# Kernel optimization log

Hardware: AMD Instinct MI355X
Metric: run time of the kernel (lower is better)

## Reference

```python
import jax, jax.numpy as jnp
import numpy as np

DIM = 1024
INTER = 512
E = 16            # n_routed_experts
TOPK = 4          # n_activated_experts
N_GROUPS = 4
TOPK_GROUPS = 2
ROUTE_SCALE = 1.0
INIT_STD = 0.02
B, S = 2, 1024


def setup_inputs() -> dict:
    key = jax.random.key(0)
    ks = jax.random.split(key, 8)
    return {
        "x": jax.random.normal(ks[0], (B, S, DIM), jnp.float32),
        "gate_w": jax.random.normal(ks[1], (E, DIM), jnp.float32) * INIT_STD,
        "gate_bias": jnp.zeros((E,), jnp.float32),
        "w1": jax.random.normal(ks[2], (E, INTER, DIM), jnp.float32) * INIT_STD,
        "w2": jax.random.normal(ks[3], (E, DIM, INTER), jnp.float32) * INIT_STD,
        "w3": jax.random.normal(ks[4], (E, INTER, DIM), jnp.float32) * INIT_STD,
        "ws1": jax.random.normal(ks[5], (INTER, DIM), jnp.float32) * INIT_STD,
        "ws2": jax.random.normal(ks[6], (DIM, INTER), jnp.float32) * INIT_STD,
        "ws3": jax.random.normal(ks[7], (INTER, DIM), jnp.float32) * INIT_STD,
    }


def reference(x, gate_w, gate_bias, w1, w2, w3, ws1, ws2, ws3):
    Bx, Sx, D = x.shape
    T = Bx * Sx
    xf = x.reshape(T, D)

    # ---- Gate: sigmoid scores + expert bias, group-limited top-k ----
    scores = jax.nn.sigmoid(xf @ gate_w.T)          # [T, E]
    original_scores = scores
    s = scores + gate_bias                          # bias only affects selection
    sg = s.reshape(T, N_GROUPS, E // N_GROUPS)
    group_scores = sg.max(axis=-1)                  # [T, G]
    _, gidx = jax.lax.top_k(group_scores, TOPK_GROUPS)
    keep = jnp.zeros((T, N_GROUPS), bool).at[jnp.arange(T)[:, None], gidx].set(True)
    s_masked = jnp.where(keep[:, :, None], sg, -jnp.inf).reshape(T, E)
    _, idx = jax.lax.top_k(s_masked, TOPK)          # [T, topk]
    weights = jnp.take_along_axis(original_scores, idx, axis=1) * ROUTE_SCALE

    # combine weights as sparse [T, E] matrix (scatter of top-k weights)
    comb = jnp.zeros((T, E), x.dtype).at[jnp.arange(T)[:, None], idx].add(weights)

    # ---- Routed experts: SwiGLU per expert, weighted combine ----
    h1 = jnp.einsum('td,eid->tei', xf, w1)          # [T, E, inter]
    h3 = jnp.einsum('td,eid->tei', xf, w3)
    h = jax.nn.silu(h1) * h3
    y = jnp.einsum('tei,edi,te->td', h, w2, comb)   # weighted combine

    # ---- Shared expert (SwiGLU MLP) ----
    z = (jax.nn.silu(xf @ ws1.T) * (xf @ ws3.T)) @ ws2.T

    return (y + z).reshape(Bx, Sx, D)
```

## Files before the change

### kernel.cpp

```cpp
#include <hip/hip_runtime.h>

#define T_TOK  2048
#define DIMD   1024
#define INTERI 512
#define NEXP   16
#define NSEG   17

typedef __bf16 bf16x8 __attribute__((ext_vector_type(8)));
typedef float  f32x4  __attribute__((ext_vector_type(4)));
typedef unsigned short u16x8 __attribute__((ext_vector_type(8)));

#define SW(row, c) ((((c) + ((row) >> 1)) & 3) * 8)

__device__ __forceinline__ unsigned short f2b(float f) {
    union { float f; unsigned int u; } c; c.f = f;
    unsigned int u = c.u;
    unsigned int r = (u + 0x7FFFu + ((u >> 16) & 1u)) >> 16;
    return (unsigned short)r;
}

__device__ __forceinline__ void glds16(const void* g, void* l) {
    __builtin_amdgcn_global_load_lds(
        (const __attribute__((address_space(1))) unsigned int*)g,
        (__attribute__((address_space(3))) unsigned int*)l,
        16, 0, 0);
}

__device__ __forceinline__ void dma_barrier() {
    asm volatile("s_waitcnt vmcnt(0)" ::: "memory");
    __syncthreads();
}

__global__ __launch_bounds__(256) void prep_kernel(
    const float* __restrict__ w1,  const float* __restrict__ w3,
    const float* __restrict__ w2,
    const float* __restrict__ ws1, const float* __restrict__ ws3,
    const float* __restrict__ ws2,
    unsigned short* __restrict__ w1b,  unsigned short* __restrict__ w3b,
    unsigned short* __restrict__ w2b,
    unsigned short* __restrict__ ws1b, unsigned short* __restrict__ ws3b,
    unsigned short* __restrict__ ws2b,
    const float* __restrict__ x, const float* __restrict__ gw,
    const float* __restrict__ gb,
    unsigned* __restrict__ sel, float4* __restrict__ selw,
    unsigned short* __restrict__ xb)
{
    const int b = blockIdx.x;
    if (b >= 512) {
        int g = (b - 512) * 256 + threadIdx.x;
        const float* s; unsigned short* d; int i;
        if      (g < 524288)  { s = w1;  d = w1b;  i = g; }
        else if (g < 1048576) { s = w3;  d = w3b;  i = g - 524288; }
        else if (g < 1572864) { s = w2;  d = w2b;  i = g - 1048576; }
        else if (g < 1605632) { s = ws1; d = ws1b; i = g - 1572864; }
        else if (g < 1638400) { s = ws3; d = ws3b; i = g - 1605632; }
        else                  { s = ws2; d = ws2b; i = g - 1638400; }
        const f32x4* sp = (const f32x4*)s;
        f32x4 v0 = __builtin_nontemporal_load(&sp[4 * i]);
        f32x4 v1 = __builtin_nontemporal_load(&sp[4 * i + 1]);
        f32x4 v2 = __builtin_nontemporal_load(&sp[4 * i + 2]);
        f32x4 v3 = __builtin_nontemporal_load(&sp[4 * i + 3]);
        u16x8 o0, o1;
        o0[0] = f2b(v0[0]); o0[1] = f2b(v0[1]); o0[2] = f2b(v0[2]); o0[3] = f2b(v0[3]);
        o0[4] = f2b(v1[0]); o0[5] = f2b(v1[1]); o0[6] = f2b(v1[2]); o0[7] = f2b(v1[3]);
        o1[0] = f2b(v2[0]); o1[1] = f2b(v2[1]); o1[2] = f2b(v2[2]); o1[3] = f2b(v2[3]);
        o1[4] = f2b(v3[0]); o1[5] = f2b(v3[1]); o1[6] = f2b(v3[2]); o1[7] = f2b(v3[3]);
        ((u16x8*)d)[2 * i]     = o0;
        ((u16x8*)d)[2 * i + 1] = o1;
        return;
    }
    int tok  = b * 4 + (threadIdx.x >> 6);
    int lane = threadIdx.x & 63;
    const float* xp = x + (size_t)tok * DIMD;
    float xv[16];
#pragma unroll
    for (int j = 0; j < 16; ++j) xv[j] = xp[j * 64 + lane];

    unsigned short* xbp = xb + (size_t)tok * DIMD;
#pragma unroll
    for (int j = 0; j < 16; ++j) xbp[j * 64 + lane] = f2b(xv[j]);

    float sc[16];
#pragma unroll
    for (int e = 0; e < 16; ++e) {
        const float* gwe = gw + e * DIMD;
        float p0 = 0.f, p1 = 0.f;
#pragma unroll
        for (int j = 0; j < 16; j += 2) {
            p0 += xv[j]     * gwe[j * 64 + lane];
            p1 += xv[j + 1] * gwe[(j + 1) * 64 + lane];
        }
        float p = p0 + p1;
#pragma unroll
        for (int o = 32; o; o >>= 1) p += __shfl_xor(p, o, 64);
        sc[e] = p;
    }
    if (lane != 0) return;

    float orig[16], s[16];
#pragma unroll
    for (int e = 0; e < 16; ++e) {
        orig[e] = 1.f / (1.f + expf(-sc[e]));
        s[e] = orig[e] + gb[e];
    }
    float gmax[4];
#pragma unroll
    for (int g = 0; g < 4; ++g) {
        float m = s[4 * g];
        for (int j = 1; j < 4; ++j) m = fmaxf(m, s[4 * g + j]);
        gmax[g] = m;
    }
    int g0 = 0;
    for (int g = 1; g < 4; ++g) if (gmax[g] > gmax[g0]) g0 = g;
    int g1 = -1;
    for (int g = 0; g < 4; ++g) { if (g == g0) continue; if (g1 < 0 || gmax[g] > gmax[g1]) g1 = g; }
    unsigned keep = (0xFu << (4 * g0)) | (0xFu << (4 * g1));
    unsigned used = 0;
    unsigned pk = 0;
    float w4[4];
    for (int j = 0; j < 4; ++j) {
        int best = -1;
        for (int e = 0; e < 16; ++e) {
            if (!((keep >> e) & 1u) || ((used >> e) & 1u)) continue;
            if (best < 0 || s[e] > s[best]) best = e;
        }
        used |= 1u << best;
        pk |= ((unsigned)best) << (4 * j);
        w4[j] = orig[best];
    }
    sel[tok] = pk;
    selw[tok] = make_float4(w4[0], w4[1], w4[2], w4[3]);
}

__global__ __launch_bounds__(256) void build_lists_kernel(
    const unsigned* __restrict__ sel, const float4* __restrict__ selw,
    int* __restrict__ counts, int* __restrict__ lst, float* __restrict__ lstw)
{
    const int e    = blockIdx.x;
    const int tid  = threadIdx.x;
    const int wave = tid >> 6;
    const int lane = tid & 63;

    __shared__ int wsum[4];
    __shared__ int basev;
    if (tid == 0) basev = 0;
    __syncthreads();

    for (int c = 0; c < T_TOK / 256; ++c) {
        int t = c * 256 + tid;
        unsigned s = sel[t];
        int match = -1;
#pragma unroll
        for (int j = 0; j < 4; ++j)
            if (((s >> (4 * j)) & 15u) == (unsigned)e) match = j;
        unsigned long long m = __ballot(match >= 0);
        int wpre = __popcll(m & ((1ull << lane) - 1ull));
        if (lane == 0) wsum[wave] = __popcll(m);
        __syncthreads();
        int pre = basev;
        for (int wv = 0; wv < wave; ++wv) pre += wsum[wv];
        if (match >= 0) {
            int pos = pre + wpre;
            lst [e * T_TOK + pos] = t | (match << 16);
            const float* wp = (const float*)&selw[t];
            lstw[e * T_TOK + pos] = wp[match];
        }
        __syncthreads();
        if (tid == 0) basev += wsum[0] + wsum[1] + wsum[2] + wsum[3];
        __syncthreads();
    }
    if (tid == 0) counts[e] = basev;
}

__global__ __launch_bounds__(256, 2) void gemm1_kernel(
    const unsigned short* __restrict__ xb,
    const unsigned short* __restrict__ w1b,
    const unsigned short* __restrict__ w3b,
    const unsigned short* __restrict__ ws1b,
    const unsigned short* __restrict__ ws3b,
    const int* __restrict__ counts,
    const int* __restrict__ lst,
    unsigned short* __restrict__ H)
{
    int b = blockIdx.x;
    int seg, mt, nt;
    if (b < 1024) {
        int xcd = b & 7, slot = b >> 3;
        seg = xcd + 8 * (slot >> 6);
        int tile = slot & 63;
        mt = tile >> 2; nt = tile & 3;
    } else {
        seg = NEXP;
        int tile = b - 1024;
        mt = tile >> 2; nt = tile & 3;
    }
    const int n_e = (seg == NEXP) ? T_TOK : counts[seg];
    const int m0  = mt * 128;
    if (m0 >= n_e) return;
    const int n0  = nt * 128;

    const unsigned short* w1p = (seg == NEXP) ? ws1b : w1b + (size_t)seg * INTERI * DIMD;
    const unsigned short* w3p = (seg == NEXP) ? ws3b : w3b + (size_t)seg * INTERI * DIMD;
    const int* lste = lst + seg * T_TOK;

    __shared__ __align__(16) unsigned short lA [2][128][32];
    __shared__ __align__(16) unsigned short lB1[2][128][32];
    __shared__ __align__(16) unsigned short lB3[2][128][32];

    const int tid  = threadIdx.x;
    const int wave = tid >> 6;
    const int lane = tid & 63;
    const int quad = lane >> 4;
    const int lrow = lane & 15;

    const int lr  = lane >> 2;
    const int lsl = lane & 3;
    const int r0  = wave * 32 + lr, r1 = r0 + 16;
    const int c0  = (lsl - (r0 >> 1)) & 3;
    const int c1  = (lsl - (r1 >> 1)) & 3;
    int ga0 = m0 + r0; if (ga0 > n_e - 1) ga0 = n_e - 1;
    int ga1 = m0 + r1; if (ga1 > n_e - 1) ga1 = n_e - 1;
    const int tA0 = (seg == NEXP) ? ga0 : (lste[ga0] & 0xFFFF);
    const int tA1 = (seg == NEXP) ? ga1 : (lste[ga1] & 0xFFFF);
    const unsigned short* pA0  = xb  + (size_t)tA0 * DIMD + c0 * 8;
    const unsigned short* pA1  = xb  + (size_t)tA1 * DIMD + c1 * 8;
    const unsigned short* pB10 = w1p + (size_t)(n0 + r0) * DIMD + c0 * 8;
    const unsigned short* pB11 = w1p + (size_t)(n0 + r1) * DIMD + c1 * 8;
    const unsigned short* pB30 = w3p + (size_t)(n0 + r0) * DIMD + c0 * 8;
    const unsigned short* pB31 = w3p + (size_t)(n0 + r1) * DIMD + c1 * 8;

#define G1STAGE(k0) do { \
    glds16(pA0  + (k0),      &lA [0][wave * 32][0]); \
    glds16(pA0  + (k0) + 32, &lA [1][wave * 32][0]); \
    glds16(pA1  + (k0),      &lA [0][wave * 32 + 16][0]); \
    glds16(pA1  + (k0) + 32, &lA [1][wave * 32 + 16][0]); \
    glds16(pB10 + (k0),      &lB1[0][wave * 32][0]); \
    glds16(pB10 + (k0) + 32, &lB1[1][wave * 32][0]); \
    glds16(pB11 + (k0),      &lB1[0][wave * 32 + 16][0]); \
    glds16(pB11 + (k0) + 32, &lB1[1][wave * 32 + 16][0]); \
    glds16(pB30 + (k0),      &lB3[0][wave * 32][0]); \
    glds16(pB30 + (k0) + 32, &lB3[1][wave * 32][0]); \
    glds16(pB31 + (k0),      &lB3[0][wave * 32 + 16][0]); \
    glds16(pB31 + (k0) + 32, &lB3[1][wave * 32 + 16][0]); \
} while (0)

    f32x4 acc1[4][4], acc3[4][4];
    const f32x4 zero = {0.f, 0.f, 0.f, 0.f};
#pragma unroll
    for (int i = 0; i < 4; ++i)
#pragma unroll
        for (int j = 0; j < 4; ++j) { acc1[i][j] = zero; acc3[i][j] = zero; }

    const int wm = (wave & 1) * 64;
    const int wn = (wave >> 1) * 64;

    const int NK = DIMD / 64;
    for (int it = 0; it < NK; ++it) {
        G1STAGE(it * 64);
        dma_barrier();
#pragma unroll
        for (int kk = 0; kk < 2; ++kk) {
            bf16x8 a[4], bv[4];
#pragma unroll
            for (int t = 0; t < 4; ++t) {
                int rr = wm + t * 16 + lrow;
                a[t] = *(const bf16x8*)&lA[kk][rr][SW(rr, quad)];
            }
#pragma unroll
            for (int t = 0; t < 4; ++t) {
                int rc = wn + t * 16 + lrow;
                bv[t] = *(const bf16x8*)&lB1[kk][rc][SW(rc, quad)];
            }
#pragma unroll
            for (int i = 0; i < 4; ++i)
#pragma unroll
                for (int j = 0; j < 4; ++j)
                    acc1[i][j] = __builtin_amdgcn_mfma_f32_16x16x32_bf16(a[i], bv[j], acc1[i][j], 0, 0, 0);
#pragma unroll
            for (int t = 0; t < 4; ++t) {
                int rc = wn + t * 16 + lrow;
                bv[t] = *(const bf16x8*)&lB3[kk][rc][SW(rc, quad)];
            }
#pragma unroll
            for (int i = 0; i < 4; ++i)
#pragma unroll
                for (int j = 0; j < 4; ++j)
                    acc3[i][j] = __builtin_amdgcn_mfma_f32_16x16x32_bf16(a[i], bv[j], acc3[i][j], 0, 0, 0);
        }
        __syncthreads();
    }
#undef G1STAGE

    unsigned short* Hseg = H + (size_t)seg * T_TOK * INTERI;
#pragma unroll
    for (int i = 0; i < 4; ++i) {
        int rbase = m0 + wm + i * 16 + quad * 4;
#pragma unroll
        for (int r = 0; r < 4; ++r) {
            int row = rbase + r;
            if (row >= n_e) continue;
            unsigned short* hrow = Hseg + (size_t)row * INTERI + n0 + wn + lrow;
#pragma unroll
            for (int j = 0; j < 4; ++j) {
                float v1 = acc1[i][j][r];
                float v3 = acc3[i][j][r];
                float hv = (v1 / (1.f + __expf(-v1))) * v3;
                hrow[j * 16] = f2b(hv);
            }
        }
    }
}

__global__ __launch_bounds__(256, 2) void gemm2_kernel(
    const unsigned short* __restrict__ H,
    const unsigned short* __restrict__ w2b,
    const unsigned short* __restrict__ ws2b,
    const int* __restrict__ counts,
    const int* __restrict__ lst,
    const float* __restrict__ lstw,
    float* __restrict__ P)
{
    int b = blockIdx.x;
    int seg, mt, nt;
    if (b < 2048) {
        int xcd = b & 7, slot = b >> 3;
        seg = xcd + 8 * (slot >> 7);
        int tile = slot & 127;
        mt = tile >> 3; nt = tile & 7;
    } else {
        seg = NEXP;
        int tile = b - 2048;
        mt = tile >> 3; nt = tile & 7;
    }
    const int n_e = (seg == NEXP) ? T_TOK : counts[seg];
    const int m0  = mt * 128;
    if (m0 >= n_e) return;
    const int n0  = nt * 128;

    const unsigned short* w2p  = (seg == NEXP) ? ws2b : w2b + (size_t)seg * DIMD * INTERI;
    const unsigned short* Hseg = H + (size_t)seg * T_TOK * INTERI;

    __shared__ __align__(16) unsigned short lA[2][128][32];
    __shared__ __align__(16) unsigned short lB[2][128][32];

    const int tid  = threadIdx.x;
    const int wave = tid >> 6;
    const int lane = tid & 63;
    const int quad = lane >> 4;
    const int lrow = lane & 15;

    const int lr  = lane >> 2;
    const int lsl = lane & 3;
    const int r0  = wave * 32 + lr, r1 = r0 + 16;
    const int c0  = (lsl - (r0 >> 1)) & 3;
    const int c1  = (lsl - (r1 >> 1)) & 3;
    int ga0 = m0 + r0; if (ga0 > n_e - 1) ga0 = n_e - 1;
    int ga1 = m0 + r1; if (ga1 > n_e - 1) ga1 = n_e - 1;
    const unsigned short* pA0 = Hseg + (size_t)ga0 * INTERI + c0 * 8;
    const unsigned short* pA1 = Hseg + (size_t)ga1 * INTERI + c1 * 8;
    const unsigned short* pB0 = w2p + (size_t)(n0 + r0) * INTERI + c0 * 8;
    const unsigned short* pB1 = w2p + (size_t)(n0 + r1) * INTERI + c1 * 8;

#define G2STAGE(k0) do { \
    glds16(pA0 + (k0),      &lA[0][wave * 32][0]); \
    glds16(pA0 + (k0) + 32, &lA[1][wave * 32][0]); \
    glds16(pA1 + (k0),      &lA[0][wave * 32 + 16][0]); \
    glds16(pA1 + (k0) + 32, &lA[1][wave * 32 + 16][0]); \
    glds16(pB0 + (k0),      &lB[0][wave * 32][0]); \
    glds16(pB0 + (k0) + 32, &lB[1][wave * 32][0]); \
    glds16(pB1 + (k0),      &lB[0][wave * 32 + 16][0]); \
    glds16(pB1 + (k0) + 32, &lB[1][wave * 32 + 16][0]); \
} while (0)

    f32x4 acc[4][4];
    const f32x4 zero = {0.f, 0.f, 0.f, 0.f};
#pragma unroll
    for (int i = 0; i < 4; ++i)
#pragma unroll
        for (int j = 0; j < 4; ++j) acc[i][j] = zero;

    const int wm = (wave & 1) * 64;
    const int wn = (wave >> 1) * 64;

    const int NK = INTERI / 64;
    for (int it = 0; it < NK; ++it) {
        G2STAGE(it * 64);
        dma_barrier();
#pragma unroll
        for (int kk = 0; kk < 2; ++kk) {
            bf16x8 a[4], bv[4];
#pragma unroll
            for (int t = 0; t < 4; ++t) {
                int rr = wm + t * 16 + lrow;
                a[t] = *(const bf16x8*)&lA[kk][rr][SW(rr, quad)];
            }
#pragma unroll
            for (int t = 0; t < 4; ++t) {
                int rc = wn + t * 16 + lrow;
                bv[t] = *(const bf16x8*)&lB[kk][rc][SW(rc, quad)];
            }
#pragma unroll
            for (int i = 0; i < 4; ++i)
#pragma unroll
                for (int j = 0; j < 4; ++j)
                    acc[i][j] = __builtin_amdgcn_mfma_f32_16x16x32_bf16(a[i], bv[j], acc[i][j], 0, 0, 0);
        }
        __syncthreads();
    }
#undef G2STAGE

#pragma unroll
    for (int i = 0; i < 4; ++i) {
        int rbase = m0 + wm + i * 16 + quad * 4;
#pragma unroll
        for (int r = 0; r < 4; ++r) {
            int row = rbase + r;
            if (row >= n_e) continue;
            int tok, slot; float wt;
            if (seg == NEXP) { tok = row; slot = 4; wt = 1.f; }
            else {
                int ent = lst[seg * T_TOK + row];
                tok = ent & 0xFFFF; slot = ent >> 16;
                wt = lstw[seg * T_TOK + row];
            }
            float* prow = P + ((size_t)slot * T_TOK + tok) * DIMD + n0 + wn + lrow;
#pragma unroll
            for (int j = 0; j < 4; ++j)
                prow[j * 16] = wt * acc[i][j][r];
        }
    }
}

__global__ __launch_bounds__(256) void combine_kernel(
    const float4* __restrict__ P, float4* __restrict__ y)
{
    const int i = blockIdx.x * 256 + threadIdx.x;
    const size_t plane = (size_t)T_TOK * DIMD / 4;
    float4 a = P[i];
    float4 b = P[plane + i];
    float4 c = P[2 * plane + i];
    float4 d = P[3 * plane + i];
    float4 e = P[4 * plane + i];
    float4 o;
    o.x = a.x + b.x + c.x + d.x + e.x;
    o.y = a.y + b.y + c.y + d.y + e.y;
    o.z = a.z + b.z + c.z + d.z + e.z;
    o.w = a.w + b.w + c.w + d.w + e.w;
    y[i] = o;
}

extern "C" void kernel_launch(void* const* d_in, const int* in_sizes, int n_in,
                              void* d_out, int out_size, void* d_ws, size_t ws_size,
                              hipStream_t stream)
{
    const float* x   = (const float*)d_in[0];
    const float* gw  = (const float*)d_in[1];
    const float* gb  = (const float*)d_in[2];
    const float* w1  = (const float*)d_in[3];
    const float* w2  = (const float*)d_in[4];
    const float* w3  = (const float*)d_in[5];
    const float* ws1 = (const float*)d_in[6];
    const float* ws2 = (const float*)d_in[7];
    const float* ws3 = (const float*)d_in[8];

    char* base = (char*)d_ws;
    size_t off = 0;
    auto alloc = [&](size_t bytes) {
        char* q = base + off; off += (bytes + 255) & ~(size_t)255; return q;
    };
    unsigned short* xb   = (unsigned short*)alloc((size_t)T_TOK * DIMD * 2);
    unsigned short* w1b  = (unsigned short*)alloc((size_t)NEXP * INTERI * DIMD * 2);
    unsigned short* w3b  = (unsigned short*)alloc((size_t)NEXP * INTERI * DIMD * 2);
    unsigned short* w2b  = (unsigned short*)alloc((size_t)NEXP * DIMD * INTERI * 2);
    unsigned short* ws1b = (unsigned short*)alloc((size_t)INTERI * DIMD * 2);
    unsigned short* ws3b = (unsigned short*)alloc((size_t)INTERI * DIMD * 2);
    unsigned short* ws2b = (unsigned short*)alloc((size_t)DIMD * INTERI * 2);
    unsigned short* Hb   = (unsigned short*)alloc((size_t)NSEG * T_TOK * INTERI * 2);
    int*            cnts = (int*)alloc(NEXP * 4);
    int*            lstp = (int*)alloc((size_t)NEXP * T_TOK * 4);
    float*          lstw = (float*)alloc((size_t)NEXP * T_TOK * 4);
    unsigned*       selp = (unsigned*)alloc((size_t)T_TOK * 4);
    float4*         selw = (float4*)alloc((size_t)T_TOK * 16);
    float*          Pb   = (float*)alloc((size_t)5 * T_TOK * DIMD * 4);

    prep_kernel<<<7040, 256, 0, stream>>>(w1, w3, w2, ws1, ws3, ws2,
                                          w1b, w3b, w2b, ws1b, ws3b, ws2b,
                                          x, gw, gb, selp, selw, xb);
    build_lists_kernel<<<NEXP, 256, 0, stream>>>(selp, selw, cnts, lstp, lstw);
    gemm1_kernel<<<1088, 256, 0, stream>>>(xb, w1b, w3b, ws1b, ws3b, cnts, lstp, Hb);
    gemm2_kernel<<<2176, 256, 0, stream>>>(Hb, w2b, ws2b, cnts, lstp, lstw, Pb);
    combine_kernel<<<(T_TOK * DIMD / 4) / 256, 256, 0, stream>>>((const float4*)Pb, (float4*)d_out);
}
```

Measured before the change: 233.4 us.

## Double-buffer LDS tiles in both expert GEMM kernels to overlap loads with MFMA

Both GEMM kernels now prefetch the next K-slice into an alternate LDS buffer while computing on the current one, and the trailing __syncthreads per iteration is removed. The first GEMM halves its K-step to 32 so the double buffer fits in the same LDS footprint. The second GEMM doubles its LDS allocation to hold two 64-wide stages. This aims to hide global-to-LDS latency behind matrix work. It risks more barrier iterations in GEMM1, higher LDS use lowering occupancy in GEMM2, and a possible race if dma_barrier alone does not stop waves from overwriting a buffer that others are still reading.

```diff
diff --git a/kernel.cpp b/kernel.cpp
--- a/kernel.cpp
+++ b/kernel.cpp
@@ -229,19 +229,13 @@
     const unsigned short* pB30 = w3p + (size_t)(n0 + r0) * DIMD + c0 * 8;
     const unsigned short* pB31 = w3p + (size_t)(n0 + r1) * DIMD + c1 * 8;
 
-#define G1STAGE(k0) do { \
-    glds16(pA0  + (k0),      &lA [0][wave * 32][0]); \
-    glds16(pA0  + (k0) + 32, &lA [1][wave * 32][0]); \
-    glds16(pA1  + (k0),      &lA [0][wave * 32 + 16][0]); \
-    glds16(pA1  + (k0) + 32, &lA [1][wave * 32 + 16][0]); \
-    glds16(pB10 + (k0),      &lB1[0][wave * 32][0]); \
-    glds16(pB10 + (k0) + 32, &lB1[1][wave * 32][0]); \
-    glds16(pB11 + (k0),      &lB1[0][wave * 32 + 16][0]); \
-    glds16(pB11 + (k0) + 32, &lB1[1][wave * 32 + 16][0]); \
-    glds16(pB30 + (k0),      &lB3[0][wave * 32][0]); \
-    glds16(pB30 + (k0) + 32, &lB3[1][wave * 32][0]); \
-    glds16(pB31 + (k0),      &lB3[0][wave * 32 + 16][0]); \
-    glds16(pB31 + (k0) + 32, &lB3[1][wave * 32 + 16][0]); \
+#define G1STAGE(buf, k0) do { \
+    glds16(pA0  + (k0), &lA [buf][wave * 32][0]); \
+    glds16(pA1  + (k0), &lA [buf][wave * 32 + 16][0]); \
+    glds16(pB10 + (k0), &lB1[buf][wave * 32][0]); \
+    glds16(pB11 + (k0), &lB1[buf][wave * 32 + 16][0]); \
+    glds16(pB30 + (k0), &lB3[buf][wave * 32][0]); \
+    glds16(pB31 + (k0), &lB3[buf][wave * 32 + 16][0]); \
 } while (0)
 
     f32x4 acc1[4][4], acc3[4][4];
@@ -254,40 +248,38 @@
     const int wm = (wave & 1) * 64;
     const int wn = (wave >> 1) * 64;
 
-    const int NK = DIMD / 64;
+    const int NK = DIMD / 32;
+    G1STAGE(0, 0);
     for (int it = 0; it < NK; ++it) {
-        G1STAGE(it * 64);
+        const int cur = it & 1;
         dma_barrier();
-#pragma unroll
-        for (int kk = 0; kk < 2; ++kk) {
-            bf16x8 a[4], bv[4];
-#pragma unroll
-            for (int t = 0; t < 4; ++t) {
-                int rr = wm + t * 16 + lrow;
-                a[t] = *(const bf16x8*)&lA[kk][rr][SW(rr, quad)];
-            }
-#pragma unroll
-            for (int t = 0; t < 4; ++t) {
-                int rc = wn + t * 16 + lrow;
-                bv[t] = *(const bf16x8*)&lB1[kk][rc][SW(rc, quad)];
-            }
-#pragma unroll
-            for (int i = 0; i < 4; ++i)
-#pragma unroll
-                for (int j = 0; j < 4; ++j)
-                    acc1[i][j] = __builtin_amdgcn_mfma_f32_16x16x32_bf16(a[i], bv[j], acc1[i][j], 0, 0, 0);
-#pragma unroll
-            for (int t = 0; t < 4; ++t) {
-                int rc = wn + t * 16 + lrow;
-                bv[t] = *(const bf16x8*)&lB3[kk][rc][SW(rc, quad)];
-            }
-#pragma unroll
-            for (int i = 0; i < 4; ++i)
-#pragma unroll
-                for (int j = 0; j < 4; ++j)
-                    acc3[i][j] = __builtin_amdgcn_mfma_f32_16x16x32_bf16(a[i], bv[j], acc3[i][j], 0, 0, 0);
-        }
-        __syncthreads();
+        if (it + 1 < NK) G1STAGE(cur ^ 1, (it + 1) * 32);
+        bf16x8 a[4], bv[4];
+#pragma unroll
+        for (int t = 0; t < 4; ++t) {
+            int rr = wm + t * 16 + lrow;
+            a[t] = *(const bf16x8*)&lA[cur][rr][SW(rr, quad)];
+        }
+#pragma unroll
+        for (int t = 0; t < 4; ++t) {
+            int rc = wn + t * 16 + lrow;
+            bv[t] = *(const bf16x8*)&lB1[cur][rc][SW(rc, quad)];
+        }
+#pragma unroll
+        for (int i = 0; i < 4; ++i)
+#pragma unroll
+            for (int j = 0; j < 4; ++j)
+                acc1[i][j] = __builtin_amdgcn_mfma_f32_16x16x32_bf16(a[i], bv[j], acc1[i][j], 0, 0, 0);
+#pragma unroll
+        for (int t = 0; t < 4; ++t) {
+            int rc = wn + t * 16 + lrow;
+            bv[t] = *(const bf16x8*)&lB3[cur][rc][SW(rc, quad)];
+        }
+#pragma unroll
+        for (int i = 0; i < 4; ++i)
+#pragma unroll
+            for (int j = 0; j < 4; ++j)
+                acc3[i][j] = __builtin_amdgcn_mfma_f32_16x16x32_bf16(a[i], bv[j], acc3[i][j], 0, 0, 0);
     }
 #undef G1STAGE
 
@@ -340,8 +332,8 @@
     const unsigned short* w2p  = (seg == NEXP) ? ws2b : w2b + (size_t)seg * DIMD * INTERI;
     const unsigned short* Hseg = H + (size_t)seg * T_TOK * INTERI;
 
-    __shared__ __align__(16) unsigned short lA[2][128][32];
-    __shared__ __align__(16) unsigned short lB[2][128][32];
+    __shared__ __align__(16) unsigned short lA[2][2][128][32];
+    __shared__ __align__(16) unsigned short lB[2][2][128][32];
 
     const int tid  = threadIdx.x;
     const int wave = tid >> 6;
@@ -361,15 +353,15 @@
     const unsigned short* pB0 = w2p + (size_t)(n0 + r0) * INTERI + c0 * 8;
     const unsigned short* pB1 = w2p + (size_t)(n0 + r1) * INTERI + c1 * 8;
 
-#define G2STAGE(k0) do { \
-    glds16(pA0 + (k0),      &lA[0][wave * 32][0]); \
-    glds16(pA0 + (k0) + 32, &lA[1][wave * 32][0]); \
-    glds16(pA1 + (k0),      &lA[0][wave * 32 + 16][0]); \
-    glds16(pA1 + (k0) + 32, &lA[1][wave * 32 + 16][0]); \
-    glds16(pB0 + (k0),      &lB[0][wave * 32][0]); \
-    glds16(pB0 + (k0) + 32, &lB[1][wave * 32][0]); \
-    glds16(pB1 + (k0),      &lB[0][wave * 32 + 16][0]); \
-    glds16(pB1 + (k0) + 32, &lB[1][wave * 32 + 16][0]); \
+#define G2STAGE(buf, k0) do { \
+    glds16(pA0 + (k0),      &lA[buf][0][wave * 32][0]); \
+    glds16(pA0 + (k0) + 32, &lA[buf][1][wave * 32][0]); \
+    glds16(pA1 + (k0),      &lA[buf][0][wave * 32 + 16][0]); \
+    glds16(pA1 + (k0) + 32, &lA[buf][1][wave * 32 + 16][0]); \
+    glds16(pB0 + (k0),      &lB[buf][0][wave * 32][0]); \
+    glds16(pB0 + (k0) + 32, &lB[buf][1][wave * 32][0]); \
+    glds16(pB1 + (k0),      &lB[buf][0][wave * 32 + 16][0]); \
+    glds16(pB1 + (k0) + 32, &lB[buf][1][wave * 32 + 16][0]); \
 } while (0)
 
     f32x4 acc[4][4];
@@ -383,21 +375,23 @@
     const int wn = (wave >> 1) * 64;
 
     const int NK = INTERI / 64;
+    G2STAGE(0, 0);
     for (int it = 0; it < NK; ++it) {
-        G2STAGE(it * 64);
+        const int cur = it & 1;
         dma_barrier();
+        if (it + 1 < NK) G2STAGE(cur ^ 1, (it + 1) * 64);
 #pragma unroll
         for (int kk = 0; kk < 2; ++kk) {
             bf16x8 a[4], bv[4];
 #pragma unroll
             for (int t = 0; t < 4; ++t) {
                 int rr = wm + t * 16 + lrow;
-                a[t] = *(const bf16x8*)&lA[kk][rr][SW(rr, quad)];
+                a[t] = *(const bf16x8*)&lA[cur][kk][rr][SW(rr, quad)];
             }
 #pragma unroll
             for (int t = 0; t < 4; ++t) {
                 int rc = wn + t * 16 + lrow;
-                bv[t] = *(const bf16x8*)&lB[kk][rc][SW(rc, quad)];
+                bv[t] = *(const bf16x8*)&lB[cur][kk][rc][SW(rc, quad)];
             }
 #pragma unroll
             for (int i = 0; i < 4; ++i)
@@ -405,7 +399,6 @@
                 for (int j = 0; j < 4; ++j)
                     acc[i][j] = __builtin_amdgcn_mfma_f32_16x16x32_bf16(a[i], bv[j], acc[i][j], 0, 0, 0);
         }
-        __syncthreads();
     }
 #undef G2STAGE
 
```

Measured after the change: 247.2 us. +5.9%, slower.

## Replace partial-output planes and combine kernel with atomic accumulation into output

Applied to the files above, without the earlier changes.

gemm2 now adds its weighted results straight into the output with float atomic adds, so the five-plane partial buffer and the separate combine kernel are gone. The output is zeroed by extra blocks in the prep kernel. This drops a kernel launch and the write and reread of five full fp32 planes (about 40 MB). In exchange it adds atomic traffic in the gemm2 epilogue, with up to five adds per output element, and the summation order becomes nondeterministic.

```diff
diff --git a/kernel.cpp b/kernel.cpp
--- a/kernel.cpp
+++ b/kernel.cpp
@@ -43,11 +43,12 @@
     const float* __restrict__ x, const float* __restrict__ gw,
     const float* __restrict__ gb,
     unsigned* __restrict__ sel, float4* __restrict__ selw,
-    unsigned short* __restrict__ xb)
+    unsigned short* __restrict__ xb,
+    float4* __restrict__ yzero)
 {
     const int b = blockIdx.x;
-    if (b >= 512) {
-        int g = (b - 512) * 256 + threadIdx.x;
+    if (b >= 2560) {
+        int g = (b - 2560) * 256 + threadIdx.x;
         const float* s; unsigned short* d; int i;
         if      (g < 524288)  { s = w1;  d = w1b;  i = g; }
         else if (g < 1048576) { s = w3;  d = w3b;  i = g - 524288; }
@@ -67,6 +68,12 @@
         o1[4] = f2b(v3[0]); o1[5] = f2b(v3[1]); o1[6] = f2b(v3[2]); o1[7] = f2b(v3[3]);
         ((u16x8*)d)[2 * i]     = o0;
         ((u16x8*)d)[2 * i + 1] = o1;
+        return;
+    }
+    if (b >= 512) {
+        int i = (b - 512) * 256 + threadIdx.x;
+        float4 z; z.x = 0.f; z.y = 0.f; z.z = 0.f; z.w = 0.f;
+        yzero[i] = z;
         return;
     }
     int tok  = b * 4 + (threadIdx.x >> 6);
@@ -318,7 +325,7 @@
     const int* __restrict__ counts,
     const int* __restrict__ lst,
     const float* __restrict__ lstw,
-    float* __restrict__ P)
+    float* __restrict__ y)
 {
     int b = blockIdx.x;
     int seg, mt, nt;
@@ -416,37 +423,19 @@
         for (int r = 0; r < 4; ++r) {
             int row = rbase + r;
             if (row >= n_e) continue;
-            int tok, slot; float wt;
-            if (seg == NEXP) { tok = row; slot = 4; wt = 1.f; }
+            int tok; float wt;
+            if (seg == NEXP) { tok = row; wt = 1.f; }
             else {
                 int ent = lst[seg * T_TOK + row];
-                tok = ent & 0xFFFF; slot = ent >> 16;
-                wt = lstw[seg * T_TOK + row];
-            }
-            float* prow = P + ((size_t)slot * T_TOK + tok) * DIMD + n0 + wn + lrow;
+                tok = ent & 0xFFFF;
+                wt  = lstw[seg * T_TOK + row];
+            }
+            float* yrow = y + (size_t)tok * DIMD + n0 + wn + lrow;
 #pragma unroll
             for (int j = 0; j < 4; ++j)
-                prow[j * 16] = wt * acc[i][j][r];
-        }
-    }
-}
-
-__global__ __launch_bounds__(256) void combine_kernel(
-    const float4* __restrict__ P, float4* __restrict__ y)
-{
-    const int i = blockIdx.x * 256 + threadIdx.x;
-    const size_t plane = (size_t)T_TOK * DIMD / 4;
-    float4 a = P[i];
-    float4 b = P[plane + i];
-    float4 c = P[2 * plane + i];
-    float4 d = P[3 * plane + i];
-    float4 e = P[4 * plane + i];
-    float4 o;
-    o.x = a.x + b.x + c.x + d.x + e.x;
-    o.y = a.y + b.y + c.y + d.y + e.y;
-    o.z = a.z + b.z + c.z + d.z + e.z;
-    o.w = a.w + b.w + c.w + d.w + e.w;
-    y[i] = o;
+                unsafeAtomicAdd(&yrow[j * 16], wt * acc[i][j][r]);
+        }
+    }
 }
 
 extern "C" void kernel_launch(void* const* d_in, const int* in_sizes, int n_in,
@@ -481,13 +470,12 @@
     float*          lstw = (float*)alloc((size_t)NEXP * T_TOK * 4);
     unsigned*       selp = (unsigned*)alloc((size_t)T_TOK * 4);
     float4*         selw = (float4*)alloc((size_t)T_TOK * 16);
-    float*          Pb   = (float*)alloc((size_t)5 * T_TOK * DIMD * 4);
-
-    prep_kernel<<<7040, 256, 0, stream>>>(w1, w3, w2, ws1, ws3, ws2,
+
+    prep_kernel<<<9088, 256, 0, stream>>>(w1, w3, w2, ws1, ws3, ws2,
                                           w1b, w3b, w2b, ws1b, ws3b, ws2b,
-                                          x, gw, gb, selp, selw, xb);
+                                          x, gw, gb, selp, selw, xb,
+                                          (float4*)d_out);
     build_lists_kernel<<<NEXP, 256, 0, stream>>>(selp, selw, cnts, lstp, lstw);
     gemm1_kernel<<<1088, 256, 0, stream>>>(xb, w1b, w3b, ws1b, ws3b, cnts, lstp, Hb);
-    gemm2_kernel<<<2176, 256, 0, stream>>>(Hb, w2b, ws2b, cnts, lstp, lstw, Pb);
-    combine_kernel<<<(T_TOK * DIMD / 4) / 256, 256, 0, stream>>>((const float4*)Pb, (float4*)d_out);
-}
+    gemm2_kernel<<<2176, 256, 0, stream>>>(Hb, w2b, ws2b, cnts, lstp, lstw, (float*)d_out);
+}
```

New measurement: 249.3 us. +6.8%, slower.
